# Kernel optimization log

Hardware: AMD Instinct MI355X
Metric: run time of the kernel (lower is better)

## Reference

```python
import jax, jax.numpy as jnp
import numpy as np

N_NODES = 100000
N_EDGES = 3200000
D_FEAT = 256
UNITS = 256


def setup_inputs() -> dict:
    key = jax.random.key(0)
    k1, k2, k3, k4, k5 = jax.random.split(key, 5)
    X = jax.random.normal(k1, (N_NODES, D_FEAT), dtype=jnp.float32)
    edge_row = jax.random.randint(k2, (N_EDGES,), 0, N_NODES, dtype=jnp.int64 if jax.config.read('jax_enable_x64') else jnp.int32)
    edge_col = jax.random.randint(k3, (N_EDGES,), 0, N_NODES, dtype=edge_row.dtype)
    edge_val = jax.random.uniform(k4, (N_EDGES,), dtype=jnp.float32)
    W = jax.random.normal(k5, (D_FEAT, UNITS), dtype=jnp.float32) * (1.0 / np.sqrt(D_FEAT))
    b = jnp.zeros((UNITS,), dtype=jnp.float32)
    return {"X": X, "edge_row": edge_row, "edge_col": edge_col,
            "edge_val": edge_val, "W": W, "b": b}


def reference(X, edge_row, edge_col, edge_val, W, b):
    # h = X @ W  (dense GEMM)  [N, units]
    h = X @ W
    # out = A @ h (sparse COO SpMM): out[i] = sum_e val[e] * h[col[e]] for row[e]==i
    msgs = edge_val[:, None] * h[edge_col]          # [E, units] gather + scale
    out = jax.ops.segment_sum(msgs, edge_row, num_segments=X.shape[0])
    out = out + b                                    # bias_add
    return jax.nn.relu(out)                          # activation
```

## Files before the change

kernel.cpp:

```cpp
#include <hip/hip_runtime.h>
#include <hip/hip_bf16.h>

#define N_NODES 100000
#define N_EDGES 3200000
#define D_FEAT  256
#define UNITS   256

#define BROWS   128
#define NB      782
#define NCHUNK  256
#define EPB     (N_EDGES / NCHUNK)
#define MAXB    6144

using frag_ab = __attribute__((ext_vector_type(8))) short;
using frag_cd = __attribute__((ext_vector_type(4))) float;

__device__ __forceinline__ unsigned short f2bf(float f) {
    union { float f; unsigned int i; } c; c.f = f;
    unsigned int r = c.i + 0x7FFF + ((c.i >> 16) & 1);
    return (unsigned short)(r >> 16);
}
__device__ __forceinline__ float h2f(unsigned short u) {
    _Float16 h; __builtin_memcpy(&h, &u, 2); return (float)h;
}
__device__ __forceinline__ unsigned short f2h(float f) {
    _Float16 h = (_Float16)f; unsigned short u; __builtin_memcpy(&u, &h, 2); return u;
}

__global__ __launch_bounds__(256) void convert_wt(const float* __restrict__ W,
                                                  unsigned short* __restrict__ Wt) {
    const int n = blockIdx.x, k = threadIdx.x;
    Wt[n * 256 + k] = f2bf(W[k * 256 + n]);
}

__global__ __launch_bounds__(256) void gemm_mfma(const float* __restrict__ X,
                                                 const unsigned short* __restrict__ Wt,
                                                 unsigned short* __restrict__ hb) {
    __shared__ unsigned short As[128 * 32];
    __shared__ unsigned short Bs[128 * 32];
    const int t    = threadIdx.x;
    const int lane = t & 63;
    const int wave = t >> 6;
    const int wm   = (wave >> 1) * 64;
    const int wn   = (wave & 1) * 64;
    const int rowBase = blockIdx.y * 128;
    const int colBase = blockIdx.x * 128;
    const int lr = lane & 15, lq = lane >> 4;

    frag_cd acc[4][4];
    #pragma unroll
    for (int i = 0; i < 4; ++i)
        #pragma unroll
        for (int j = 0; j < 4; ++j)
            acc[i][j] = (frag_cd){0.f, 0.f, 0.f, 0.f};

    for (int k0 = 0; k0 < D_FEAT; k0 += 32) {
        #pragma unroll
        for (int cc = 0; cc < 4; ++cc) {
            const int c = t + cc * 256;
            const int r = c >> 3, fo = (c & 7) * 4;
            const int grow = min(rowBase + r, N_NODES - 1);
            const float4 xv = *(const float4*)(X + (size_t)grow * D_FEAT + k0 + fo);
            ushort4 o;
            o.x = f2bf(xv.x); o.y = f2bf(xv.y); o.z = f2bf(xv.z); o.w = f2bf(xv.w);
            *(ushort4*)(As + r * 32 + fo) = o;
        }
        #pragma unroll
        for (int cc = 0; cc < 2; ++cc) {
            const int c = t + cc * 256;
            const int r = c >> 2, ko = (c & 3) * 8;
            *(uint4*)(Bs + c * 8) =
                *(const uint4*)(Wt + (size_t)(colBase + r) * 256 + k0 + ko);
        }
        __syncthreads();

        frag_ab a[4], b[4];
        #pragma unroll
        for (int i = 0; i < 4; ++i)
            a[i] = *(const frag_ab*)(As + (wm + i * 16 + lr) * 32 + lq * 8);
        #pragma unroll
        for (int j = 0; j < 4; ++j)
            b[j] = *(const frag_ab*)(Bs + (wn + j * 16 + lr) * 32 + lq * 8);

        #pragma unroll
        for (int i = 0; i < 4; ++i)
            #pragma unroll
            for (int j = 0; j < 4; ++j)
                acc[i][j] = __builtin_amdgcn_mfma_f32_16x16x32_bf16(
                    a[i], b[j], acc[i][j], 0, 0, 0);
        __syncthreads();
    }

    #pragma unroll
    for (int i = 0; i < 4; ++i) {
        #pragma unroll
        for (int rr = 0; rr < 4; ++rr) {
            const int row = rowBase + wm + i * 16 + lq * 4 + rr;
            if (row < N_NODES) {
                #pragma unroll
                for (int j = 0; j < 4; ++j) {
                    hb[(size_t)row * 256 + colBase + wn + j * 16 + lr] =
                        f2h(acc[i][j][rr]);
                }
            }
        }
    }
}

__global__ __launch_bounds__(256) void quantize_h(const unsigned short* __restrict__ hb,
                                                  unsigned char* __restrict__ hq,
                                                  float* __restrict__ hscale) {
    const int r    = blockIdx.x * 4 + (threadIdx.x >> 6);
    const int lane = threadIdx.x & 63;
    const ushort4 hv = *(const ushort4*)(hb + (size_t)r * 256 + lane * 4);
    const float f0 = h2f(hv.x), f1 = h2f(hv.y), f2 = h2f(hv.z), f3 = h2f(hv.w);
    float m = fmaxf(fmaxf(fabsf(f0), fabsf(f1)), fmaxf(fabsf(f2), fabsf(f3)));
    #pragma unroll
    for (int o = 32; o; o >>= 1) m = fmaxf(m, __shfl_xor(m, o));
    const float inv = (m > 0.f) ? 127.f / m : 0.f;
    const int q0 = (int)rintf(f0 * inv);
    const int q1 = (int)rintf(f1 * inv);
    const int q2 = (int)rintf(f2 * inv);
    const int q3 = (int)rintf(f3 * inv);
    const unsigned int w = ((unsigned)q0 & 0xFF) | (((unsigned)q1 & 0xFF) << 8) |
                           (((unsigned)q2 & 0xFF) << 16) | (((unsigned)q3 & 0xFF) << 24);
    *(unsigned int*)(hq + (size_t)r * 256 + lane * 4) = w;
    if (lane == 0) hscale[r] = m * (1.f / 127.f);
}

__global__ __launch_bounds__(256) void hist_kernel(const int* __restrict__ erow,
                                                   int* __restrict__ hist_g) {
    __shared__ int h[NB];
    const int t = threadIdx.x;
    const int b = blockIdx.x;
    for (int i = t; i < NB; i += 256) h[i] = 0;
    __syncthreads();
    const int base_e = b * EPB;
    for (int i = t; i < EPB; i += 256)
        atomicAdd(&h[erow[base_e + i] >> 7], 1);
    __syncthreads();
    for (int i = t; i < NB; i += 256)
        hist_g[b * NB + i] = h[i];
}

__global__ __launch_bounds__(256) void scan_buckets(const int* __restrict__ hist_g,
                                                    int* __restrict__ cum,
                                                    int* __restrict__ total) {
    const int k = blockIdx.x, t = threadIdx.x;
    __shared__ int p[256];
    const int v = hist_g[t * NB + k];
    p[t] = v;
    __syncthreads();
    for (int d = 1; d < 256; d <<= 1) {
        const int u = (t >= d) ? p[t - d] : 0;
        __syncthreads();
        p[t] += u;
        __syncthreads();
    }
    cum[t * NB + k] = p[t] - v;
    if (t == 255) total[k] = p[255];
}

__global__ __launch_bounds__(1024) void scan_base(const int* __restrict__ total,
                                                  int* __restrict__ base) {
    const int t = threadIdx.x;
    __shared__ int p[1024];
    const int v = (t < NB) ? total[t] : 0;
    p[t] = v;
    __syncthreads();
    for (int d = 1; d < 1024; d <<= 1) {
        const int u = (t >= d) ? p[t - d] : 0;
        __syncthreads();
        p[t] += u;
        __syncthreads();
    }
    if (t < NB) base[t] = p[t] - v;
    if (t == NB - 1) base[NB] = p[t];
}

__global__ __launch_bounds__(256) void scatter_binned(const int* __restrict__ erow,
                                                      const int* __restrict__ ecol,
                                                      const float* __restrict__ eval,
                                                      const float* __restrict__ hscale,
                                                      const int* __restrict__ cum,
                                                      const int* __restrict__ base,
                                                      uint2* __restrict__ binned) {
    __shared__ int cur[NB];
    const int t = threadIdx.x;
    const int b = blockIdx.x;
    for (int i = t; i < NB; i += 256)
        cur[i] = base[i] + cum[b * NB + i];
    __syncthreads();
    const int base_e = b * EPB;
    for (int i = t; i < EPB; i += 256) {
        const int e = base_e + i;
        const int r = erow[e];
        const int c = ecol[e];
        const float v = eval[e] * hscale[c];
        const int k = r >> 7, rl = r & 127;
        const int pos = atomicAdd(&cur[k], 1);
        binned[pos] = make_uint2(((unsigned)rl << 17) | (unsigned)c,
                                 __float_as_uint(v));
    }
}

__global__ __launch_bounds__(256) void sort_local(const uint2* __restrict__ binned,
                                                  const int* __restrict__ base,
                                                  const int* __restrict__ total,
                                                  uint2* __restrict__ sorted,
                                                  int* __restrict__ offs) {
    __shared__ uint2 buf[MAXB];
    __shared__ int lh[BROWS], loff[BROWS], lcur[BROWS];
    const int k = blockIdx.x, t = threadIdx.x;
    const int s = base[k];
    const int cnt = min(total[k], MAXB);

    if (t < BROWS) lh[t] = 0;
    __syncthreads();
    for (int i = t; i < cnt; i += 256)
        atomicAdd(&lh[binned[s + i].x >> 17], 1);
    __syncthreads();
    if (t < BROWS) loff[t] = lh[t];
    __syncthreads();
    for (int d = 1; d < BROWS; d <<= 1) {
        const int u = (t >= d && t < BROWS) ? loff[t - d] : 0;
        __syncthreads();
        if (t < BROWS) loff[t] += u;
        __syncthreads();
    }
    if (t < BROWS) lcur[t] = loff[t] - lh[t];
    __syncthreads();
    for (int i = t; i < cnt; i += 256) {
        const uint2 eo = binned[s + i];
        const int rl = eo.x >> 17;
        const int p = atomicAdd(&lcur[rl], 1);
        buf[p] = make_uint2(eo.x & 0x1FFFF, eo.y);
    }
    __syncthreads();
    for (int i = t; i < cnt; i += 256)
        sorted[s + i] = buf[i];
    const int rowBase = k * BROWS;
    if (t < BROWS && rowBase + t < N_NODES)
        offs[rowBase + t] = s + (loff[t] - lh[t]);
    if (t == 0 && k == NB - 1)
        offs[N_NODES] = N_EDGES;
}

__global__ __launch_bounds__(64) void spmm_rows(const int* __restrict__ offs,
                                                const uint2* __restrict__ sorted,
                                                const unsigned char* __restrict__ hq,
                                                const float* __restrict__ bias,
                                                float* __restrict__ out) {
    const int r = blockIdx.x;
    const int lane = threadIdx.x;
    __shared__ uint2 le[64];
    int s = offs[r];
    const int e = offs[r + 1];
    float a0 = 0.f, a1 = 0.f, a2 = 0.f, a3 = 0.f;

    while (s < e) {
        const int cnt = min(64, e - s);
        if (lane < cnt) {
            uint2 v = sorted[s + lane];
            v.x &= 0x1FFFF;
            le[lane] = v;
        }
        __syncthreads();
        #pragma unroll 4
        for (int j = 0; j < cnt; ++j) {
            const uint2 cv = le[j];
            const float v = __uint_as_float(cv.y);
            const unsigned int w = *(const unsigned int*)(hq + (size_t)cv.x * 256 + lane * 4);
            a0 += v * (float)((int)(signed char)( w        & 0xFF));
            a1 += v * (float)((int)(signed char)((w >> 8)  & 0xFF));
            a2 += v * (float)((int)(signed char)((w >> 16) & 0xFF));
            a3 += v * (float)((int)(signed char)( w >> 24        ));
        }
        __syncthreads();
        s += cnt;
    }

    const float4 b4 = *(const float4*)(bias + lane * 4);
    float4 o;
    o.x = fmaxf(a0 + b4.x, 0.f);
    o.y = fmaxf(a1 + b4.y, 0.f);
    o.z = fmaxf(a2 + b4.z, 0.f);
    o.w = fmaxf(a3 + b4.w, 0.f);
    *(float4*)(out + (size_t)r * 256 + lane * 4) = o;
}

extern "C" void kernel_launch(void* const* d_in, const int* in_sizes, int n_in,
                              void* d_out, int out_size, void* d_ws, size_t ws_size,
                              hipStream_t stream) {
    const float* X    = (const float*)d_in[0];
    const int*   erow = (const int*)  d_in[1];
    const int*   ecol = (const int*)  d_in[2];
    const float* evalv= (const float*)d_in[3];
    const float* W    = (const float*)d_in[4];
    const float* bias = (const float*)d_in[5];
    float* out = (float*)d_out;

    char* ws = (char*)d_ws;
    size_t off = 0;
    auto alloc = [&](size_t bytes) {
        void* p = ws + off;
        off += (bytes + 255) & ~(size_t)255;
        return p;
    };
    unsigned short* Wt     = (unsigned short*)alloc((size_t)D_FEAT * UNITS * 2);
    unsigned short* hb     = (unsigned short*)alloc((size_t)N_NODES * UNITS * 2);
    unsigned char*  hq     = (unsigned char*) alloc((size_t)N_NODES * UNITS);
    float*          hscale = (float*)         alloc((size_t)N_NODES * 4);
    uint2*          binned = (uint2*)         alloc((size_t)N_EDGES * 8);
    uint2*          sorted = (uint2*)         alloc((size_t)N_EDGES * 8);
    int*            hist_g = (int*)           alloc((size_t)NCHUNK * NB * 4);
    int*            cum    = (int*)           alloc((size_t)NCHUNK * NB * 4);
    int*            total  = (int*)           alloc((size_t)NB * 4);
    int*            basep  = (int*)           alloc((size_t)(NB + 1) * 4);
    int*            offs   = (int*)           alloc((size_t)(N_NODES + 1) * 4);

    convert_wt<<<UNITS, 256, 0, stream>>>(W, Wt);
    gemm_mfma<<<dim3(UNITS / 128, (N_NODES + 127) / 128), 256, 0, stream>>>(X, Wt, hb);
    quantize_h<<<N_NODES / 4, 256, 0, stream>>>(hb, hq, hscale);
    hist_kernel<<<NCHUNK, 256, 0, stream>>>(erow, hist_g);
    scan_buckets<<<NB, 256, 0, stream>>>(hist_g, cum, total);
    scan_base<<<1, 1024, 0, stream>>>(total, basep);
    scatter_binned<<<NCHUNK, 256, 0, stream>>>(erow, ecol, evalv, hscale, cum, basep, binned);
    sort_local<<<NB, 256, 0, stream>>>(binned, basep, total, sorted, offs);
    spmm_rows<<<N_NODES, 64, 0, stream>>>(offs, sorted, hq, bias, out);
}
```

Baseline: 471.5 us.

## Fuse int8 row quantization into GEMM epilogue with full-width tiles

The GEMM now computes all 256 output columns per block (512 threads, 8 waves), so each block holds complete rows. It can then find per-row absmax via shuffles and shared atomics and write int8 values and scales directly. This removes the fp16 intermediate buffer and the separate quantize kernel, cutting one 51MB write and read plus a launch. X is also read once instead of twice across column blocks. The cost is larger blocks with more LDS use and an extra synchronization-heavy epilogue. Quantization now works from fp32 accumulators instead of fp16-rounded values.

```diff
diff --git a/kernel.cpp b/kernel.cpp
--- a/kernel.cpp
+++ b/kernel.cpp
@@ -20,12 +20,6 @@
     unsigned int r = c.i + 0x7FFF + ((c.i >> 16) & 1);
     return (unsigned short)(r >> 16);
 }
-__device__ __forceinline__ float h2f(unsigned short u) {
-    _Float16 h; __builtin_memcpy(&h, &u, 2); return (float)h;
-}
-__device__ __forceinline__ unsigned short f2h(float f) {
-    _Float16 h = (_Float16)f; unsigned short u; __builtin_memcpy(&u, &h, 2); return u;
-}
 
 __global__ __launch_bounds__(256) void convert_wt(const float* __restrict__ W,
                                                   unsigned short* __restrict__ Wt) {
@@ -33,19 +27,25 @@
     Wt[n * 256 + k] = f2bf(W[k * 256 + n]);
 }
 
-__global__ __launch_bounds__(256) void gemm_mfma(const float* __restrict__ X,
-                                                 const unsigned short* __restrict__ Wt,
-                                                 unsigned short* __restrict__ hb) {
-    __shared__ unsigned short As[128 * 32];
-    __shared__ unsigned short Bs[128 * 32];
+__global__ __launch_bounds__(512) void gemm_q(const float* __restrict__ X,
+                                              const unsigned short* __restrict__ Wt,
+                                              unsigned char* __restrict__ hq,
+                                              float* __restrict__ hscale) {
+    __shared__ __align__(16) unsigned char smem[32768];
+    __shared__ int rowmax_i[128];
+    unsigned short* As = (unsigned short*)smem;
+    unsigned short* Bs = (unsigned short*)(smem + 8192);
+    unsigned char*  qbuf = smem;
+
     const int t    = threadIdx.x;
     const int lane = t & 63;
     const int wave = t >> 6;
-    const int wm   = (wave >> 1) * 64;
-    const int wn   = (wave & 1) * 64;
-    const int rowBase = blockIdx.y * 128;
-    const int colBase = blockIdx.x * 128;
+    const int wm   = (wave >> 2) * 64;
+    const int wn   = (wave & 3) * 64;
+    const int rowBase = blockIdx.x * 128;
     const int lr = lane & 15, lq = lane >> 4;
+
+    if (t < 128) rowmax_i[t] = 0;
 
     frag_cd acc[4][4];
     #pragma unroll
@@ -56,8 +56,8 @@
 
     for (int k0 = 0; k0 < D_FEAT; k0 += 32) {
         #pragma unroll
-        for (int cc = 0; cc < 4; ++cc) {
-            const int c = t + cc * 256;
+        for (int cc = 0; cc < 2; ++cc) {
+            const int c = t + cc * 512;
             const int r = c >> 3, fo = (c & 7) * 4;
             const int grow = min(rowBase + r, N_NODES - 1);
             const float4 xv = *(const float4*)(X + (size_t)grow * D_FEAT + k0 + fo);
@@ -67,10 +67,9 @@
         }
         #pragma unroll
         for (int cc = 0; cc < 2; ++cc) {
-            const int c = t + cc * 256;
-            const int r = c >> 2, ko = (c & 3) * 8;
+            const int c = t + cc * 512;
             *(uint4*)(Bs + c * 8) =
-                *(const uint4*)(Wt + (size_t)(colBase + r) * 256 + k0 + ko);
+                *(const uint4*)(Wt + (size_t)(c >> 2) * 256 + k0 + (c & 3) * 8);
         }
         __syncthreads();
 
@@ -91,41 +90,59 @@
         __syncthreads();
     }
 
-    #pragma unroll
-    for (int i = 0; i < 4; ++i) {
+    float pm[4][4];
+    #pragma unroll
+    for (int i = 0; i < 4; ++i)
         #pragma unroll
         for (int rr = 0; rr < 4; ++rr) {
-            const int row = rowBase + wm + i * 16 + lq * 4 + rr;
-            if (row < N_NODES) {
-                #pragma unroll
-                for (int j = 0; j < 4; ++j) {
-                    hb[(size_t)row * 256 + colBase + wn + j * 16 + lr] =
-                        f2h(acc[i][j][rr]);
-                }
+            float m = fabsf(acc[i][0][rr]);
+            m = fmaxf(m, fabsf(acc[i][1][rr]));
+            m = fmaxf(m, fabsf(acc[i][2][rr]));
+            m = fmaxf(m, fabsf(acc[i][3][rr]));
+            pm[i][rr] = m;
+        }
+    #pragma unroll
+    for (int o = 1; o <= 8; o <<= 1)
+        #pragma unroll
+        for (int i = 0; i < 4; ++i)
+            #pragma unroll
+            for (int rr = 0; rr < 4; ++rr)
+                pm[i][rr] = fmaxf(pm[i][rr], __shfl_xor(pm[i][rr], o));
+    if (lr == 0) {
+        #pragma unroll
+        for (int i = 0; i < 4; ++i)
+            #pragma unroll
+            for (int rr = 0; rr < 4; ++rr)
+                atomicMax(&rowmax_i[wm + i * 16 + lq * 4 + rr],
+                          __float_as_int(pm[i][rr]));
+    }
+    __syncthreads();
+
+    #pragma unroll
+    for (int i = 0; i < 4; ++i)
+        #pragma unroll
+        for (int rr = 0; rr < 4; ++rr) {
+            const int row = wm + i * 16 + lq * 4 + rr;
+            const float m = __int_as_float(rowmax_i[row]);
+            const float inv = (m > 0.f) ? 127.f / m : 0.f;
+            #pragma unroll
+            for (int j = 0; j < 4; ++j) {
+                const int q = (int)rintf(acc[i][j][rr] * inv);
+                qbuf[row * 256 + wn + j * 16 + lr] = (unsigned char)(signed char)q;
             }
         }
-    }
-}
-
-__global__ __launch_bounds__(256) void quantize_h(const unsigned short* __restrict__ hb,
-                                                  unsigned char* __restrict__ hq,
-                                                  float* __restrict__ hscale) {
-    const int r    = blockIdx.x * 4 + (threadIdx.x >> 6);
-    const int lane = threadIdx.x & 63;
-    const ushort4 hv = *(const ushort4*)(hb + (size_t)r * 256 + lane * 4);
-    const float f0 = h2f(hv.x), f1 = h2f(hv.y), f2 = h2f(hv.z), f3 = h2f(hv.w);
-    float m = fmaxf(fmaxf(fabsf(f0), fabsf(f1)), fmaxf(fabsf(f2), fabsf(f3)));
-    #pragma unroll
-    for (int o = 32; o; o >>= 1) m = fmaxf(m, __shfl_xor(m, o));
-    const float inv = (m > 0.f) ? 127.f / m : 0.f;
-    const int q0 = (int)rintf(f0 * inv);
-    const int q1 = (int)rintf(f1 * inv);
-    const int q2 = (int)rintf(f2 * inv);
-    const int q3 = (int)rintf(f3 * inv);
-    const unsigned int w = ((unsigned)q0 & 0xFF) | (((unsigned)q1 & 0xFF) << 8) |
-                           (((unsigned)q2 & 0xFF) << 16) | (((unsigned)q3 & 0xFF) << 24);
-    *(unsigned int*)(hq + (size_t)r * 256 + lane * 4) = w;
-    if (lane == 0) hscale[r] = m * (1.f / 127.f);
+    __syncthreads();
+
+    #pragma unroll
+    for (int cc = 0; cc < 4; ++cc) {
+        const int c = t + cc * 512;
+        const int row = c >> 4, fo = (c & 15) * 16;
+        const int grow = rowBase + row;
+        if (grow < N_NODES)
+            *(uint4*)(hq + (size_t)grow * 256 + fo) = *(const uint4*)(qbuf + row * 256 + fo);
+    }
+    if (t < 128 && rowBase + t < N_NODES)
+        hscale[rowBase + t] = __int_as_float(rowmax_i[t]) * (1.f / 127.f);
 }
 
 __global__ __launch_bounds__(256) void hist_kernel(const int* __restrict__ erow,
@@ -308,7 +325,6 @@
         return p;
     };
     unsigned short* Wt     = (unsigned short*)alloc((size_t)D_FEAT * UNITS * 2);
-    unsigned short* hb     = (unsigned short*)alloc((size_t)N_NODES * UNITS * 2);
     unsigned char*  hq     = (unsigned char*) alloc((size_t)N_NODES * UNITS);
     float*          hscale = (float*)         alloc((size_t)N_NODES * 4);
     uint2*          binned = (uint2*)         alloc((size_t)N_EDGES * 8);
@@ -320,8 +336,7 @@
     int*            offs   = (int*)           alloc((size_t)(N_NODES + 1) * 4);
 
     convert_wt<<<UNITS, 256, 0, stream>>>(W, Wt);
-    gemm_mfma<<<dim3(UNITS / 128, (N_NODES + 127) / 128), 256, 0, stream>>>(X, Wt, hb);
-    quantize_h<<<N_NODES / 4, 256, 0, stream>>>(hb, hq, hscale);
+    gemm_q<<<NB, 512, 0, stream>>>(X, Wt, hq, hscale);
     hist_kernel<<<NCHUNK, 256, 0, stream>>>(erow, hist_g);
     scan_buckets<<<NB, 256, 0, stream>>>(hist_g, cum, total);
     scan_base<<<1, 1024, 0, stream>>>(total, basep);
```

Result: faster. 450.5 us (-4.5%).
